# Performance work log

Hardware: AMD Instinct MI355X
Metric: run time of the kernel (lower is better)

## Reference

```python
import jax, jax.numpy as jnp
import numpy as np

B, N, D, H, W, OUT = 2, 2048, 128, 8, 4, 256

def setup_inputs() -> dict:
    key = jax.random.key(0)
    ks = jax.random.split(key, 8)
    s = 0.02
    return {
        "nodefeatures": jax.random.normal(ks[0], (B, N, D), jnp.float32),
        "nodeadj": jax.random.uniform(ks[1], (B, N, N, W), jnp.float32),
        "Wq": jax.random.normal(ks[2], (H, D, D), jnp.float32) * s,
        "bq": jnp.zeros((H, D), jnp.float32),
        "Wk": jax.random.normal(ks[3], (H, D, D), jnp.float32) * s,
        "bk": jnp.zeros((H, D), jnp.float32),
        "Wv": jax.random.normal(ks[4], (H, D, D), jnp.float32) * s,
        "bv": jnp.zeros((H, D), jnp.float32),
        "Wout": jax.random.normal(ks[5], (H * D, OUT), jnp.float32) * s,
        "bout": jnp.zeros((OUT,), jnp.float32),
    }

def reference(nodefeatures, nodeadj, Wq, bq, Wk, bk, Wv, bv, Wout, bout):
    # Per-head linear projections, all heads at once: [B,H,N,D]
    q = jnp.einsum('bnd,hde->bhne', nodefeatures, Wq) + bq[None, :, None, :]
    k = jnp.einsum('bnd,hde->bhne', nodefeatures, Wk) + bk[None, :, None, :]
    v = jnp.einsum('bnd,hde->bhne', nodefeatures, Wv) + bv[None, :, None, :]
    # Original scales by k.shape[1]**0.5 == sqrt(N) (node count, not head dim)
    scores = jnp.einsum('bhnd,bhmd->bhnm', q, k) / jnp.sqrt(jnp.asarray(N, q.dtype))
    # (scores[...,None] * nodeadj).sum(-1) == scores * nodeadj.sum(-1)
    scores = scores * nodeadj.sum(-1)[:, None, :, :]  # [B,H,N,N]
    attn = jax.nn.softmax(scores, axis=-1)  # torch softmax(dim=2) on [B,N,N] == key axis
    o = jnp.einsum('bhnm,bhmd->bhnd', attn, v)
    o = jnp.moveaxis(o, 1, 2).reshape(B, N, H * D)  # concat heads along feature dim
    return o @ Wout + bout
```

## Files before the change

### kernel.cpp

```cpp
#include <hip/hip_runtime.h>
#include <hip/hip_bf16.h>

#define BB 2
#define NN 2048
#define DD 128
#define HH 8
#define OUTD 256
#define SCALE 0.022097086912079612f

typedef __bf16 bf16x8 __attribute__((ext_vector_type(8)));
typedef float f32x4 __attribute__((ext_vector_type(4)));
typedef _Float16 f16x4 __attribute__((ext_vector_type(4)));

__device__ __forceinline__ unsigned short f2bf(float f) {
    union { float f; unsigned int u; } v; v.f = f;
    unsigned int r = (v.u + 0x7FFFu + ((v.u >> 16) & 1u)) >> 16;
    return (unsigned short)r;
}
__device__ __forceinline__ float bf2f(unsigned short s) {
    union { unsigned int u; float f; } v; v.u = ((unsigned int)s) << 16;
    return v.f;
}
__device__ __forceinline__ void gl_lds16(const unsigned short* g, unsigned short* l) {
    __builtin_amdgcn_global_load_lds(
        (const __attribute__((address_space(1))) unsigned int*)g,
        (__attribute__((address_space(3))) unsigned int*)l,
        16, 0, 0);
}

__global__ void prep_kernel(const float* __restrict__ X,
                            const float* __restrict__ Wq,
                            const float* __restrict__ Wk,
                            const float* __restrict__ Wv,
                            const float* __restrict__ Wout,
                            unsigned short* __restrict__ Xb,
                            unsigned short* __restrict__ WT,
                            unsigned short* __restrict__ WoutT)
{
    const int NX  = BB * NN * DD;
    const int NW  = 3 * HH * DD * DD;
    const int NWO = (HH * DD) * OUTD;
    int idx = blockIdx.x * blockDim.x + threadIdx.x;
    if (idx < NX) {
        Xb[idx] = f2bf(X[idx]);
    } else if (idx < NX + NW) {
        int i = idx - NX;
        int mat = i / (HH * DD * DD);
        int r   = i % (HH * DD * DD);
        int h = r / (DD * DD);
        int j = r % (DD * DD);
        int e = j / DD;
        int d = j % DD;
        const float* Wm = (mat == 0) ? Wq : ((mat == 1) ? Wk : Wv);
        WT[i] = f2bf(Wm[h * DD * DD + d * DD + e]);
    } else if (idx < NX + NW + NWO) {
        int i = idx - NX - NW;
        int o = i / (HH * DD);
        int k = i % (HH * DD);
        WoutT[i] = f2bf(Wout[k * OUTD + o]);
    }
}

__global__ void adjsum_kernel(const float4* __restrict__ adj, unsigned short* __restrict__ s) {
    int idx = blockIdx.x * blockDim.x + threadIdx.x;
    float4 a = adj[idx];
    s[idx] = f2bf((a.x + a.y) + (a.z + a.w));
}

__global__ __launch_bounds__(256) void proj_kernel(
    const unsigned short* __restrict__ Xb,
    const unsigned short* __restrict__ WT,
    const float* __restrict__ bq, const float* __restrict__ bk, const float* __restrict__ bv,
    unsigned short* __restrict__ Qo, unsigned short* __restrict__ Ko,
    unsigned short* __restrict__ Vt)
{
    const int mat = blockIdx.z;
    const int bh  = blockIdx.y;
    const int b = bh >> 3, h = bh & 7;
    const int n0 = blockIdx.x * 64;
    const int tid = threadIdx.x;
    const int lane = tid & 63, wv = tid >> 6;
    const int m = lane & 15, quad = lane >> 4;

    __shared__ unsigned short Wlds[128 * 136];

    const unsigned short* Wg = WT + ((size_t)mat * HH + h) * (DD * DD);
    #pragma unroll
    for (int i = tid; i < 128 * 16; i += 256) {
        int r = i >> 4, c = i & 15;
        *(uint4*)&Wlds[r * 136 + c * 8] = *(const uint4*)(Wg + r * 128 + c * 8);
    }

    const int row = n0 + wv * 16 + m;
    const unsigned short* Xr = Xb + ((size_t)b * NN + row) * DD;
    bf16x8 af[4];
    #pragma unroll
    for (int kc = 0; kc < 4; ++kc)
        af[kc] = *(const bf16x8*)(Xr + kc * 32 + quad * 8);

    __syncthreads();

    f32x4 acc[8];
    #pragma unroll
    for (int et = 0; et < 8; ++et) acc[et] = (f32x4){0.f, 0.f, 0.f, 0.f};

    #pragma unroll
    for (int kc = 0; kc < 4; ++kc) {
        #pragma unroll
        for (int et = 0; et < 8; ++et) {
            bf16x8 bfrg = *(const bf16x8*)&Wlds[(et * 16 + m) * 136 + kc * 32 + quad * 8];
            acc[et] = __builtin_amdgcn_mfma_f32_16x16x32_bf16(af[kc], bfrg, acc[et], 0, 0, 0);
        }
    }

    const float* bias = (mat == 0) ? bq : ((mat == 1) ? bk : bv);
    if (mat != 2) {
        #pragma unroll
        for (int et = 0; et < 8; ++et) {
            int e = et * 16 + m;
            float bb = bias[h * DD + e];
            #pragma unroll
            for (int reg = 0; reg < 4; ++reg) {
                int r = n0 + wv * 16 + quad * 4 + reg;
                unsigned short v16 = f2bf(acc[et][reg] + bb);
                if (mat == 0) Qo[((size_t)bh * NN + r) * DD + e] = v16;
                else          Ko[((size_t)bh * NN + r) * DD + e] = v16;
            }
        }
    } else {
        __syncthreads();
        #pragma unroll
        for (int et = 0; et < 8; ++et) {
            int e = et * 16 + m;
            float bb = bias[h * DD + e];
            #pragma unroll
            for (int reg = 0; reg < 4; ++reg)
                Wlds[(wv * 16 + quad * 4 + reg) * 136 + e] = f2bf(acc[et][reg] + bb);
        }
        __syncthreads();
        const int e = tid >> 1, nh = tid & 1;
        #pragma unroll
        for (int j = 0; j < 4; ++j) {
            unsigned short tmp[8];
            #pragma unroll
            for (int kk = 0; kk < 8; ++kk)
                tmp[kk] = Wlds[(nh * 32 + j * 8 + kk) * 136 + e];
            *(uint4*)(Vt + ((size_t)bh * DD + e) * NN + n0 + nh * 32 + j * 8) = *(uint4*)tmp;
        }
    }
}

__global__ __launch_bounds__(256, 2) void attn_kernel(
    const unsigned short* __restrict__ Q,
    const unsigned short* __restrict__ K,
    const unsigned short* __restrict__ Vt,
    const unsigned short* __restrict__ adjs,
    _Float16* __restrict__ Opart,
    float* __restrict__ Lpart)
{
    const int x = blockIdx.x;
    const int h = blockIdx.y;
    const int ks = x & 1, qt = (x >> 1) & 15, b = x >> 5;
    const int bh = b * HH + h;
    const int q0 = qt * 128;
    const int kstart = ks * 1024;
    const int tid = threadIdx.x;
    const int lane = tid & 63, wv = tid >> 6;
    const int m = lane & 15, quad = lane >> 4;

    __shared__ unsigned short Kb[2][32 * 128];
    __shared__ unsigned short Vb[2][128 * 32];
    __shared__ unsigned short Plds[4][32 * 40];

    const unsigned short* Kbase = K + (size_t)bh * NN * DD;
    const unsigned short* Vbase = Vt + (size_t)bh * DD * NN;

    bf16x8 qf[2][4];
    #pragma unroll
    for (int nq = 0; nq < 2; ++nq) {
        const unsigned short* Qr = Q + ((size_t)bh * NN + q0 + wv * 32 + nq * 16 + m) * DD;
        #pragma unroll
        for (int kc = 0; kc < 4; ++kc)
            qf[nq][kc] = *(const bf16x8*)(Qr + kc * 32 + quad * 8);
    }

    f32x4 o[2][8];
    #pragma unroll
    for (int nq = 0; nq < 2; ++nq)
        #pragma unroll
        for (int dt = 0; dt < 8; ++dt) o[nq][dt] = (f32x4){0.f, 0.f, 0.f, 0.f};
    float li[2][4] = {{0.f, 0.f, 0.f, 0.f}, {0.f, 0.f, 0.f, 0.f}};

    const unsigned short* Abase = adjs + ((size_t)b * NN + q0 + wv * 32 + quad * 4) * NN;

    const int kr4 = lane >> 4, kc16 = lane & 15;
    const int vr16 = lane >> 2, vc4 = lane & 3;

    #define STAGE(buf, kbase_)                                                              \
        {                                                                                   \
            _Pragma("unroll")                                                               \
            for (int j2 = 0; j2 < 2; ++j2) {                                                \
                const int j = wv * 2 + j2;                                                  \
                const int krow = j * 4 + kr4;                                               \
                gl_lds16(Kbase + (size_t)((kbase_) + krow) * DD + ((kc16 ^ (krow & 15)) * 8),\
                         &Kb[buf][j * 512]);                                                \
                const int vrow = j * 16 + vr16;                                             \
                gl_lds16(Vbase + (size_t)vrow * NN + (kbase_) + ((vc4 ^ ((vr16 >> 1) & 3)) * 8),\
                         &Vb[buf][j * 512]);                                                \
            }                                                                               \
        }

    STAGE(0, kstart);
    __syncthreads();

    for (int kt = 0; kt < 32; ++kt) {
        const int cb = kt & 1, nb = cb ^ 1;
        const int k0 = kstart + kt * 32;

        float ar[2][2][4];
        #pragma unroll
        for (int nq = 0; nq < 2; ++nq)
            #pragma unroll
            for (int nt = 0; nt < 2; ++nt)
                #pragma unroll
                for (int reg = 0; reg < 4; ++reg)
                    ar[nq][nt][reg] =
                        bf2f(Abase[(size_t)(nq * 16 + reg) * NN + k0 + nt * 16 + m]) * SCALE;

        if (kt + 1 < 32) STAGE(nb, k0 + 32);

        f32x4 s[2][2];
        #pragma unroll
        for (int nq = 0; nq < 2; ++nq)
            #pragma unroll
            for (int nt = 0; nt < 2; ++nt) s[nq][nt] = (f32x4){0.f, 0.f, 0.f, 0.f};
        #pragma unroll
        for (int kc = 0; kc < 4; ++kc) {
            #pragma unroll
            for (int nt = 0; nt < 2; ++nt) {
                bf16x8 kf = *(const bf16x8*)&Kb[cb][(nt * 16 + m) * 128 + (((kc * 4 + quad) ^ m) * 8)];
                s[0][nt] = __builtin_amdgcn_mfma_f32_16x16x32_bf16(qf[0][kc], kf, s[0][nt], 0, 0, 0);
                s[1][nt] = __builtin_amdgcn_mfma_f32_16x16x32_bf16(qf[1][kc], kf, s[1][nt], 0, 0, 0);
            }
        }

        #pragma unroll
        for (int nq = 0; nq < 2; ++nq) {
            #pragma unroll
            for (int nt = 0; nt < 2; ++nt) {
                #pragma unroll
                for (int reg = 0; reg < 4; ++reg) {
                    float p = __expf(s[nq][nt][reg] * ar[nq][nt][reg]);
                    li[nq][reg] += p;
                    Plds[wv][(nq * 16 + quad * 4 + reg) * 40 + nt * 16 + m] = f2bf(p);
                }
            }
        }

        bf16x8 pf[2];
        pf[0] = *(const bf16x8*)&Plds[wv][(0 * 16 + m) * 40 + quad * 8];
        pf[1] = *(const bf16x8*)&Plds[wv][(1 * 16 + m) * 40 + quad * 8];
        #pragma unroll
        for (int dt = 0; dt < 8; ++dt) {
            bf16x8 vf = *(const bf16x8*)&Vb[cb][(dt * 16 + m) * 32 + ((quad ^ ((m >> 1) & 3)) * 8)];
            o[0][dt] = __builtin_amdgcn_mfma_f32_16x16x32_bf16(pf[0], vf, o[0][dt], 0, 0, 0);
            o[1][dt] = __builtin_amdgcn_mfma_f32_16x16x32_bf16(pf[1], vf, o[1][dt], 0, 0, 0);
        }

        __syncthreads();
    }
    #undef STAGE

    #pragma unroll
    for (int nq = 0; nq < 2; ++nq) {
        #pragma unroll
        for (int reg = 0; reg < 4; ++reg) {
            float t = li[nq][reg];
            t += __shfl_xor(t, 1);
            t += __shfl_xor(t, 2);
            t += __shfl_xor(t, 4);
            t += __shfl_xor(t, 8);
            li[nq][reg] = t;
        }
        const int rbase = q0 + wv * 32 + nq * 16 + quad * 4;
        if (m == 0) {
            #pragma unroll
            for (int reg = 0; reg < 4; ++reg)
                Lpart[((size_t)ks * (BB * HH) + bh) * NN + rbase + reg] = li[nq][reg];
        }
        #pragma unroll
        for (int reg = 0; reg < 4; ++reg) {
            const size_t obase = (((size_t)ks * (BB * HH) + bh) * NN + rbase + reg) * DD;
            #pragma unroll
            for (int dt = 0; dt < 8; ++dt)
                Opart[obase + dt * 16 + m] = (_Float16)o[nq][dt][reg];
        }
    }
}

__global__ void combine_kernel(const _Float16* __restrict__ Op,
                               const float* __restrict__ Lp,
                               unsigned short* __restrict__ Ocat)
{
    const int SPLIT_OFF = BB * HH * NN * DD;
    int t = blockIdx.x * blockDim.x + threadIdx.x;
    int e0 = t * 4;
    int row = e0 >> 7;
    float l = 1.0f / (Lp[row] + Lp[row + BB * HH * NN]);
    f16x4 a = *(const f16x4*)(Op + e0);
    f16x4 c = *(const f16x4*)(Op + SPLIT_OFF + e0);
    int bh = row >> 11, n = row & (NN - 1);
    int b = bh >> 3, h = bh & 7;
    size_t obase = ((size_t)(b * NN + n)) * (HH * DD) + h * DD + (e0 & (DD - 1));
    unsigned short u[4];
    #pragma unroll
    for (int i = 0; i < 4; ++i)
        u[i] = f2bf(((float)a[i] + (float)c[i]) * l);
    *(ushort4*)(Ocat + obase) = *(ushort4*)u;
}

__global__ __launch_bounds__(256) void out_kernel(
    const unsigned short* __restrict__ Ocat,
    const unsigned short* __restrict__ WoutT,
    const float* __restrict__ bout,
    float* __restrict__ out)
{
    const int m0 = blockIdx.x * 64;
    const int c0 = blockIdx.y * 64;
    const int tid = threadIdx.x;
    const int lane = tid & 63, wv = tid >> 6;
    const int m = lane & 15, quad = lane >> 4;

    __shared__ unsigned short Wlds[64 * 136];

    f32x4 acc[4];
    #pragma unroll
    for (int nt = 0; nt < 4; ++nt) acc[nt] = (f32x4){0.f, 0.f, 0.f, 0.f};

    const unsigned short* Orow = Ocat + (size_t)(m0 + wv * 16 + m) * (HH * DD);

    for (int kc = 0; kc < 8; ++kc) {
        #pragma unroll
        for (int i = tid; i < 64 * 16; i += 256) {
            int r = i >> 4, c = i & 15;
            *(uint4*)&Wlds[r * 136 + c * 8] =
                *(const uint4*)(WoutT + (size_t)(c0 + r) * (HH * DD) + kc * 128 + c * 8);
        }
        __syncthreads();
        #pragma unroll
        for (int j = 0; j < 4; ++j) {
            bf16x8 afr = *(const bf16x8*)(Orow + kc * 128 + j * 32 + quad * 8);
            #pragma unroll
            for (int nt = 0; nt < 4; ++nt) {
                bf16x8 bfr = *(const bf16x8*)&Wlds[(nt * 16 + m) * 136 + j * 32 + quad * 8];
                acc[nt] = __builtin_amdgcn_mfma_f32_16x16x32_bf16(afr, bfr, acc[nt], 0, 0, 0);
            }
        }
        __syncthreads();
    }

    #pragma unroll
    for (int nt = 0; nt < 4; ++nt) {
        int oc = c0 + nt * 16 + m;
        float bb = bout[oc];
        #pragma unroll
        for (int reg = 0; reg < 4; ++reg) {
            int r = m0 + wv * 16 + quad * 4 + reg;
            out[(size_t)r * OUTD + oc] = acc[nt][reg] + bb;
        }
    }
}

extern "C" void kernel_launch(void* const* d_in, const int* in_sizes, int n_in,
                              void* d_out, int out_size, void* d_ws, size_t ws_size,
                              hipStream_t stream)
{
    const float* X    = (const float*)d_in[0];
    const float* adj  = (const float*)d_in[1];
    const float* Wq   = (const float*)d_in[2];
    const float* bq   = (const float*)d_in[3];
    const float* Wk   = (const float*)d_in[4];
    const float* bk   = (const float*)d_in[5];
    const float* Wv   = (const float*)d_in[6];
    const float* bv   = (const float*)d_in[7];
    const float* Wout = (const float*)d_in[8];
    const float* bout = (const float*)d_in[9];
    float* out = (float*)d_out;

    char* ws = (char*)d_ws;
    unsigned short* Xb    = (unsigned short*)(ws);
    unsigned short* WT    = (unsigned short*)(ws + 1048576);
    unsigned short* WoutT = (unsigned short*)(ws + 1835008);
    unsigned short* Q     = (unsigned short*)(ws + 2359296);
    unsigned short* Kp    = (unsigned short*)(ws + 10747904);
    unsigned short* Vt    = (unsigned short*)(ws + 19136512);
    unsigned short* Ocat  = (unsigned short*)(ws + 27525120);
    unsigned short* AsumB = (unsigned short*)(ws + 35913728);
    _Float16*       Opart = (_Float16*)(ws + 52690944);
    float*          Lpart = (float*)(ws);

    prep_kernel<<<4608, 256, 0, stream>>>(X, Wq, Wk, Wv, Wout, Xb, WT, WoutT);
    adjsum_kernel<<<(BB * NN * NN) / 256, 256, 0, stream>>>((const float4*)adj, AsumB);
    proj_kernel<<<dim3(NN / 64, BB * HH, 3), 256, 0, stream>>>(Xb, WT, bq, bk, bv, Q, Kp, Vt);
    attn_kernel<<<dim3(64, HH), 256, 0, stream>>>(Q, Kp, Vt, AsumB, Opart, Lpart);
    combine_kernel<<<(BB * HH * NN * DD / 4) / 256, 256, 0, stream>>>(Opart, Lpart, Ocat);
    out_kernel<<<dim3((BB * NN) / 64, OUTD / 64), 256, 0, stream>>>(Ocat, WoutT, bout, out);
}
```

Baseline: 315.9 us.

## Permute adjacency-sum layout for vectorized loads and register-prefetch it

The adjacency-sum kernel now writes each 128-key block in a permuted order, so each lane's 16 adjacency values for four 32-key tiles sit contiguously. The attention kernel reads them with 16-byte vector loads once per 128 keys and prefetches the next group into registers while computing the current one. This replaces many scattered 2-byte global loads per tile, whose latency sat on the critical path, at the cost of extra registers for the acur/anxt buffers, which could lower occupancy.

After: 349.3 us. +10.6%, slower.

```diff
diff --git a/kernel.cpp b/kernel.cpp
--- a/kernel.cpp
+++ b/kernel.cpp
@@ -11,6 +11,7 @@
 typedef __bf16 bf16x8 __attribute__((ext_vector_type(8)));
 typedef float f32x4 __attribute__((ext_vector_type(4)));
 typedef _Float16 f16x4 __attribute__((ext_vector_type(4)));
+typedef unsigned short u16x8 __attribute__((ext_vector_type(8)));
 
 __device__ __forceinline__ unsigned short f2bf(float f) {
     union { float f; unsigned int u; } v; v.f = f;
@@ -64,7 +65,9 @@
 __global__ void adjsum_kernel(const float4* __restrict__ adj, unsigned short* __restrict__ s) {
     int idx = blockIdx.x * blockDim.x + threadIdx.x;
     float4 a = adj[idx];
-    s[idx] = f2bf((a.x + a.y) + (a.z + a.w));
+    int k = idx & (NN - 1);
+    int p = (k & ~127) + ((k & 15) << 3) + (((k >> 5) & 3) << 1) + ((k >> 4) & 1);
+    s[(idx & ~(NN - 1)) | p] = f2bf((a.x + a.y) + (a.z + a.w));
 }
 
 __global__ __launch_bounds__(256) void proj_kernel(
@@ -191,7 +194,8 @@
         for (int dt = 0; dt < 8; ++dt) o[nq][dt] = (f32x4){0.f, 0.f, 0.f, 0.f};
     float li[2][4] = {{0.f, 0.f, 0.f, 0.f}, {0.f, 0.f, 0.f, 0.f}};
 
-    const unsigned short* Abase = adjs + ((size_t)b * NN + q0 + wv * 32 + quad * 4) * NN;
+    const unsigned short* Ab =
+        adjs + ((size_t)(b * NN + q0 + wv * 32 + quad * 4)) * NN + kstart + m * 8;
 
     const int kr4 = lane >> 4, kc16 = lane & 15;
     const int vr16 = lane >> 2, vc4 = lane & 3;
@@ -210,64 +214,78 @@
             }                                                                               \
         }
 
+    u16x8 acur[8], anxt[8];
+    #pragma unroll
+    for (int j = 0; j < 8; ++j)
+        acur[j] = *(const u16x8*)(Ab + ((j >> 2) * 16 + (j & 3)) * NN);
+
     STAGE(0, kstart);
     __syncthreads();
 
-    for (int kt = 0; kt < 32; ++kt) {
-        const int cb = kt & 1, nb = cb ^ 1;
-        const int k0 = kstart + kt * 32;
-
-        float ar[2][2][4];
-        #pragma unroll
-        for (int nq = 0; nq < 2; ++nq)
-            #pragma unroll
-            for (int nt = 0; nt < 2; ++nt)
+    for (int g = 0; g < 8; ++g) {
+        if (g < 7) {
+            #pragma unroll
+            for (int j = 0; j < 8; ++j)
+                anxt[j] = *(const u16x8*)(Ab + ((j >> 2) * 16 + (j & 3)) * NN + (g + 1) * 128);
+        }
+        #pragma unroll
+        for (int t = 0; t < 4; ++t) {
+            const int kt = g * 4 + t;
+            const int cb = kt & 1, nb = cb ^ 1;
+            const int k0 = kstart + kt * 32;
+
+            float ar[2][2][4];
+            #pragma unroll
+            for (int j = 0; j < 8; ++j) {
+                const int nq = j >> 2, reg = j & 3;
+                ar[nq][0][reg] = bf2f(acur[j][t * 2 + 0]) * SCALE;
+                ar[nq][1][reg] = bf2f(acur[j][t * 2 + 1]) * SCALE;
+            }
+
+            if (kt + 1 < 32) STAGE(nb, k0 + 32);
+
+            f32x4 s[2][2];
+            #pragma unroll
+            for (int nq = 0; nq < 2; ++nq)
                 #pragma unroll
-                for (int reg = 0; reg < 4; ++reg)
-                    ar[nq][nt][reg] =
-                        bf2f(Abase[(size_t)(nq * 16 + reg) * NN + k0 + nt * 16 + m]) * SCALE;
-
-        if (kt + 1 < 32) STAGE(nb, k0 + 32);
-
-        f32x4 s[2][2];
-        #pragma unroll
-        for (int nq = 0; nq < 2; ++nq)
-            #pragma unroll
-            for (int nt = 0; nt < 2; ++nt) s[nq][nt] = (f32x4){0.f, 0.f, 0.f, 0.f};
-        #pragma unroll
-        for (int kc = 0; kc < 4; ++kc) {
-            #pragma unroll
-            for (int nt = 0; nt < 2; ++nt) {
-                bf16x8 kf = *(const bf16x8*)&Kb[cb][(nt * 16 + m) * 128 + (((kc * 4 + quad) ^ m) * 8)];
-                s[0][nt] = __builtin_amdgcn_mfma_f32_16x16x32_bf16(qf[0][kc], kf, s[0][nt], 0, 0, 0);
-                s[1][nt] = __builtin_amdgcn_mfma_f32_16x16x32_bf16(qf[1][kc], kf, s[1][nt], 0, 0, 0);
-            }
-        }
-
-        #pragma unroll
-        for (int nq = 0; nq < 2; ++nq) {
-            #pragma unroll
-            for (int nt = 0; nt < 2; ++nt) {
+                for (int nt = 0; nt < 2; ++nt) s[nq][nt] = (f32x4){0.f, 0.f, 0.f, 0.f};
+            #pragma unroll
+            for (int kc = 0; kc < 4; ++kc) {
                 #pragma unroll
-                for (int reg = 0; reg < 4; ++reg) {
-                    float p = __expf(s[nq][nt][reg] * ar[nq][nt][reg]);
-                    li[nq][reg] += p;
-                    Plds[wv][(nq * 16 + quad * 4 + reg) * 40 + nt * 16 + m] = f2bf(p);
+                for (int nt = 0; nt < 2; ++nt) {
+                    bf16x8 kf = *(const bf16x8*)&Kb[cb][(nt * 16 + m) * 128 + (((kc * 4 + quad) ^ m) * 8)];
+                    s[0][nt] = __builtin_amdgcn_mfma_f32_16x16x32_bf16(qf[0][kc], kf, s[0][nt], 0, 0, 0);
+                    s[1][nt] = __builtin_amdgcn_mfma_f32_16x16x32_bf16(qf[1][kc], kf, s[1][nt], 0, 0, 0);
                 }
             }
-        }
-
-        bf16x8 pf[2];
-        pf[0] = *(const bf16x8*)&Plds[wv][(0 * 16 + m) * 40 + quad * 8];
-        pf[1] = *(const bf16x8*)&Plds[wv][(1 * 16 + m) * 40 + quad * 8];
-        #pragma unroll
-        for (int dt = 0; dt < 8; ++dt) {
-            bf16x8 vf = *(const bf16x8*)&Vb[cb][(dt * 16 + m) * 32 + ((quad ^ ((m >> 1) & 3)) * 8)];
-            o[0][dt] = __builtin_amdgcn_mfma_f32_16x16x32_bf16(pf[0], vf, o[0][dt], 0, 0, 0);
-            o[1][dt] = __builtin_amdgcn_mfma_f32_16x16x32_bf16(pf[1], vf, o[1][dt], 0, 0, 0);
-        }
-
-        __syncthreads();
+
+            #pragma unroll
+            for (int nq = 0; nq < 2; ++nq) {
+                #pragma unroll
+                for (int nt = 0; nt < 2; ++nt) {
+                    #pragma unroll
+                    for (int reg = 0; reg < 4; ++reg) {
+                        float p = __expf(s[nq][nt][reg] * ar[nq][nt][reg]);
+                        li[nq][reg] += p;
+                        Plds[wv][(nq * 16 + quad * 4 + reg) * 40 + nt * 16 + m] = f2bf(p);
+                    }
+                }
+            }
+
+            bf16x8 pf[2];
+            pf[0] = *(const bf16x8*)&Plds[wv][(0 * 16 + m) * 40 + quad * 8];
+            pf[1] = *(const bf16x8*)&Plds[wv][(1 * 16 + m) * 40 + quad * 8];
+            #pragma unroll
+            for (int dt = 0; dt < 8; ++dt) {
+                bf16x8 vf = *(const bf16x8*)&Vb[cb][(dt * 16 + m) * 32 + ((quad ^ ((m >> 1) & 3)) * 8)];
+                o[0][dt] = __builtin_amdgcn_mfma_f32_16x16x32_bf16(pf[0], vf, o[0][dt], 0, 0, 0);
+                o[1][dt] = __builtin_amdgcn_mfma_f32_16x16x32_bf16(pf[1], vf, o[1][dt], 0, 0, 0);
+            }
+
+            __syncthreads();
+        }
+        #pragma unroll
+        for (int j = 0; j < 8; ++j) acur[j] = anxt[j];
     }
     #undef STAGE
 
```
